# Kernel optimization log

Measured on AMD Instinct MI355X. Metric: run time of the kernel, lower is better.

## Reference

```python
import jax, jax.numpy as jnp
import numpy as np

V, H, L, B, S, T = 32000, 256, 4, 32, 64, 64


def setup_inputs() -> dict:
    key = jax.random.key(0)
    ks = jax.random.split(key, 16)
    sc = 0.05
    return {
        "encoder_outputs": jax.random.normal(ks[0], (B, S, H), jnp.float32),
        "encoder_hidden": jax.random.normal(ks[1], (L, B, H), jnp.float32),
        "decoder_input": jax.random.randint(ks[2], (B, T), 0, V),
        "embedding": jax.random.normal(ks[3], (V, H), jnp.float32) * sc,
        "Wa": jax.random.normal(ks[4], (H, H * L), jnp.float32) * sc,
        "bWa": jnp.zeros((H,), jnp.float32),
        "Ua": jax.random.normal(ks[5], (H, H), jnp.float32) * sc,
        "bUa": jnp.zeros((H,), jnp.float32),
        "Va": jax.random.normal(ks[6], (1, H), jnp.float32) * sc,
        "bVa": jnp.zeros((1,), jnp.float32),
        "W_ih0": jax.random.normal(ks[7], (3 * H, 2 * H), jnp.float32) * sc,
        "W_ih_rest": jax.random.normal(ks[8], (L - 1, 3 * H, H), jnp.float32) * sc,
        "W_hh": jax.random.normal(ks[9], (L, 3 * H, H), jnp.float32) * sc,
        "b_ih": jnp.zeros((L, 3 * H), jnp.float32),
        "b_hh": jnp.zeros((L, 3 * H), jnp.float32),
        "W_out": jax.random.normal(ks[10], (V, H), jnp.float32) * sc,
        "b_out": jnp.zeros((V,), jnp.float32),
    }


def _gru_cell(x, h, W_ih, W_hh, b_ih, b_hh):
    # PyTorch gate order: r, z, n
    gi = x @ W_ih.T + b_ih  # [B, 3H]
    gh = h @ W_hh.T + b_hh  # [B, 3H]
    ir, iz, inn = jnp.split(gi, 3, axis=-1)
    hr, hz, hn = jnp.split(gh, 3, axis=-1)
    r = jax.nn.sigmoid(ir + hr)
    z = jax.nn.sigmoid(iz + hz)
    n = jnp.tanh(inn + r * hn)
    return (1.0 - z) * n + z * h


def reference(encoder_outputs, encoder_hidden, decoder_input, embedding,
              Wa, bWa, Ua, bUa, Va, bVa,
              W_ih0, W_ih_rest, W_hh, b_ih, b_hh, W_out, b_out):
    keys = encoder_outputs  # [B,S,H]
    UaK = keys @ Ua.T + bUa  # precompute Ua(keys): [B,S,H]
    nlayers = W_hh.shape[0]

    def step(hidden, tok):
        # hidden: [L,B,H], tok: [B]
        emb = embedding[tok]  # [B,H]
        query = jnp.transpose(hidden, (1, 0, 2)).reshape(hidden.shape[1], -1)  # [B, L*H]
        e = jnp.tanh((query @ Wa.T + bWa)[:, None, :] + UaK)  # [B,S,H]
        scores = jnp.squeeze(e @ Va.T + bVa, -1)  # [B,S]
        w = jax.nn.softmax(scores, axis=-1)  # [B,S]
        ctx = jnp.einsum('bs,bsh->bh', w, keys)  # [B,H]
        x = jnp.concatenate([emb, ctx], axis=-1)  # [B,2H]
        new_h = []
        for l in range(nlayers):
            Wih = W_ih0 if l == 0 else W_ih_rest[l - 1]
            h_l = _gru_cell(x, hidden[l], Wih, W_hh[l], b_ih[l], b_hh[l])
            new_h.append(h_l)
            x = h_l
        logits = x @ W_out.T + b_out  # [B,V]
        return jnp.stack(new_h, 0), (logits, w)

    hidden_final, (logits_tbv, attn_tbs) = jax.lax.scan(step, encoder_hidden, decoder_input.T)
    logits = jnp.transpose(logits_tbv, (1, 0, 2))  # [B,T,V]
    attentions = jnp.transpose(attn_tbs, (1, 0, 2))  # [B,T,S]
    return jax.nn.log_softmax(logits, axis=-1), hidden_final, attentions
```

## Files before the change

### kernel.cpp

```cpp
#include <hip/hip_runtime.h>

typedef short s16x8 __attribute__((ext_vector_type(8)));
typedef float f32x4 __attribute__((ext_vector_type(4)));

static __device__ __forceinline__ unsigned short f2bf(float f){
  unsigned u = __builtin_bit_cast(unsigned, f);
  unsigned r = (u + 0x7fffu + ((u >> 16) & 1u)) >> 16;
  return (unsigned short)r;
}
static __device__ __forceinline__ float sigm(float x){
  return __builtin_amdgcn_rcpf(1.f + __expf(-x));
}
static __device__ __forceinline__ float tanh_(float x){
  float e = __expf(2.f * x);
  return 1.f - 2.f * __builtin_amdgcn_rcpf(e + 1.f);
}

__global__ void k_tr(const float* __restrict__ in, float* __restrict__ out, int R, int C, int ld){
  int i = blockIdx.x * 256 + threadIdx.x;
  if (i >= R * C) return;
  int c = i / R, r = i - c * R;
  out[i] = in[r * ld + c];
}

__global__ void k_wbpack(const float* __restrict__ W, unsigned short* __restrict__ Wb){
  int p = blockIdx.x * 256 + threadIdx.x;
  int j = p & 7, l = (p >> 3) & 63, ks = (p >> 9) & 7, nt = p >> 12;
  int v = nt * 16 + (l & 15);
  int k = ks * 32 + ((l >> 4) << 3) + j;
  Wb[p] = f2bf(W[v * 256 + k]);
}

__global__ void k_uak(const float* __restrict__ keys, const float* __restrict__ UaT,
                      const float* __restrict__ bUa, float* __restrict__ UaK){
  __shared__ float kl[256];
  int row = blockIdx.x, tid = threadIdx.x;
  kl[tid] = keys[row * 256 + tid];
  __syncthreads();
  float acc = bUa[tid];
  #pragma unroll 8
  for (int k = 0; k < 256; ++k) acc += kl[k] * UaT[k * 256 + tid];
  UaK[row * 256 + tid] = acc;
}

__global__ void k_gie(const int* __restrict__ tok, const float* __restrict__ emb,
                      const float* __restrict__ W0eT, const float* __restrict__ bih,
                      float* __restrict__ giE){
  __shared__ float el[256];
  int blk = blockIdx.x;
  int t = blk >> 5, b = blk & 31, tid = threadIdx.x;
  int tk = tok[b * 64 + t];
  el[tid] = emb[tk * 256 + tid];
  __syncthreads();
  for (int g = tid; g < 768; g += 256){
    float acc = bih[g];
    #pragma unroll 8
    for (int k = 0; k < 256; ++k) acc += el[k] * W0eT[k * 768 + g];
    giE[blk * 768 + g] = acc;
  }
}

__launch_bounds__(512)
__global__ void k_seq(const float* __restrict__ keys, const float* __restrict__ ehid,
                      const float* __restrict__ WaT, const float* __restrict__ bWa,
                      const float* __restrict__ Va, const float* __restrict__ bVa,
                      const float* __restrict__ UaK, const float* __restrict__ giE,
                      const float* __restrict__ W0cT, const float* __restrict__ WihT,
                      const float* __restrict__ WhhT, const float* __restrict__ bih,
                      const float* __restrict__ bhh,
                      unsigned short* __restrict__ Xb, float* __restrict__ outH,
                      float* __restrict__ outA)
{
  __shared__ float h[1024];
  __shared__ float vlds[256];
  __shared__ float qWp[1024];
  __shared__ float qW[256];
  __shared__ float ghA[3072];
  __shared__ float sc[64];
  __shared__ float watt[64];
  __shared__ float ctx[256];
  __shared__ float gi[768];
  __shared__ float red[1536];
  const int b = blockIdx.x;
  const int tid = threadIdx.x;

  for (int i = tid; i < 1024; i += 512) h[i] = ehid[(i >> 8) * 8192 + b * 256 + (i & 255)];
  if (tid < 256) vlds[tid] = Va[tid];
  __syncthreads();

  for (int t = 0; t < 64; ++t){
    #pragma unroll
    for (int pass = 0; pass < 2; ++pass){
      const int gidx = tid + pass * 512;
      const float* wp; int wstride, l, oo, isq;
      if (gidx < 256){
        isq = 1; l = gidx >> 6; oo = (gidx & 63) * 4;
        wp = WaT + l * 65536 + oo; wstride = 256;
      } else {
        isq = 0; int gid = gidx - 256; l = gid / 192; oo = (gid - l * 192) * 4;
        wp = WhhT + l * 196608 + oo; wstride = 768;
      }
      const float* xv = h + l * 256;
      float ax = 0.f, ay = 0.f, az = 0.f, aw = 0.f;
      #pragma unroll 8
      for (int k = 0; k < 256; ++k){
        float x = xv[k];
        float4 w = *(const float4*)(wp);
        ax += x * w.x; ay += x * w.y; az += x * w.z; aw += x * w.w;
        wp += wstride;
      }
      if (isq){
        float* d = qWp + l * 256 + oo;
        d[0] = ax; d[1] = ay; d[2] = az; d[3] = aw;
      } else {
        const float* bb = bhh + l * 768 + oo;
        float* d = ghA + l * 768 + oo;
        d[0] = ax + bb[0]; d[1] = ay + bb[1]; d[2] = az + bb[2]; d[3] = aw + bb[3];
      }
    }
    __syncthreads();
    if (tid < 256) qW[tid] = qWp[tid] + qWp[256 + tid] + qWp[512 + tid] + qWp[768 + tid] + bWa[tid];
    __syncthreads();

    {
      int s = tid >> 3, p = tid & 7;
      const float* up = UaK + ((b << 6) + s) * 256 + p * 32;
      const float* qp = qW + p * 32;
      const float* vp = vlds + p * 32;
      float acc = 0.f;
      #pragma unroll 8
      for (int i = 0; i < 32; ++i){
        float e = tanh_(qp[i] + up[i]);
        acc += vp[i] * e;
      }
      acc += __shfl_xor(acc, 1, 64);
      acc += __shfl_xor(acc, 2, 64);
      acc += __shfl_xor(acc, 4, 64);
      if (p == 0) sc[s] = acc + bVa[0];
    }
    __syncthreads();

    if (tid < 64){
      float v = sc[tid];
      float m = v;
      #pragma unroll
      for (int off = 1; off < 64; off <<= 1) m = fmaxf(m, __shfl_xor(m, off, 64));
      float e = __expf(v - m);
      float ssum = e;
      #pragma unroll
      for (int off = 1; off < 64; off <<= 1) ssum += __shfl_xor(ssum, off, 64);
      float w = e * __builtin_amdgcn_rcpf(ssum);
      watt[tid] = w;
      outA[(b * 64 + t) * 64 + tid] = w;
    }
    __syncthreads();

    {
      int o = tid & 255, p = tid >> 8;
      const float* kp = keys + (b * 64 + p * 32) * 256 + o;
      float acc = 0.f;
      #pragma unroll 8
      for (int s2 = 0; s2 < 32; ++s2) acc += watt[p * 32 + s2] * kp[s2 * 256];
      red[tid] = acc;
    }
    __syncthreads();
    if (tid < 256) ctx[tid] = red[tid] + red[256 + tid];
    __syncthreads();

    const float* giB = giE + (t * 32 + b) * 768;
    for (int l = 0; l < 4; ++l){
      const float* xv = (l == 0) ? ctx : (h + (l - 1) * 256);
      const float* wb = (l == 0) ? W0cT : (WihT + (l - 1) * 196608);
      if (tid < 384){
        int oo = (tid % 192) * 4, kp2 = tid / 192;
        const float* wp = wb + (kp2 * 128) * 768 + oo;
        const float* xp = xv + kp2 * 128;
        float ax = 0.f, ay = 0.f, az = 0.f, aw = 0.f;
        #pragma unroll 8
        for (int k = 0; k < 128; ++k){
          float x = xp[k];
          float4 w = *(const float4*)(wp);
          ax += x * w.x; ay += x * w.y; az += x * w.z; aw += x * w.w;
          wp += 768;
        }
        float* d = red + kp2 * 768 + oo;
        d[0] = ax; d[1] = ay; d[2] = az; d[3] = aw;
      }
      __syncthreads();
      for (int o = tid; o < 768; o += 512){
        float base = (l == 0) ? giB[o] : bih[l * 768 + o];
        gi[o] = base + red[o] + red[768 + o];
      }
      __syncthreads();
      if (tid < 256){
        int o = tid;
        const float* gh = ghA + l * 768;
        float r = sigm(gi[o] + gh[o]);
        float z = sigm(gi[256 + o] + gh[256 + o]);
        float n = tanh_(gi[512 + o] + r * gh[512 + o]);
        float hold = h[l * 256 + o];
        float hn = (1.f - z) * n + z * hold;
        h[l * 256 + o] = hn;
        if (l == 3) Xb[(b * 64 + t) * 256 + o] = f2bf(hn);
      }
      __syncthreads();
    }
  }
  for (int i = tid; i < 1024; i += 512) outH[(i >> 8) * 8192 + b * 256 + (i & 255)] = h[i];
}

__launch_bounds__(512)
__global__ void k_g1(const unsigned short* __restrict__ Xb, const unsigned short* __restrict__ Wb,
                     const float* __restrict__ bout, float* __restrict__ Spart)
{
  const int mt = blockIdx.x, nc = blockIdx.y;
  const int tid = threadIdx.x, lane = tid & 63, wv = tid >> 6;
  const int c = lane & 15, q = lane >> 4;
  const int r0 = mt * 64;
  s16x8 afr[4][8];
  #pragma unroll
  for (int rt = 0; rt < 4; ++rt){
    const unsigned short* xp = Xb + (r0 + rt * 16 + c) * 256 + q * 8;
    #pragma unroll
    for (int ks = 0; ks < 8; ++ks) afr[rt][ks] = *(const s16x8*)(xp + ks * 32);
  }
  float ssum[4][4];
  #pragma unroll
  for (int rt = 0; rt < 4; ++rt){ ssum[rt][0]=0.f; ssum[rt][1]=0.f; ssum[rt][2]=0.f; ssum[rt][3]=0.f; }
  const int ntEnd = nc * 250 + 250;
  for (int nt = nc * 250 + wv; nt < ntEnd; nt += 8){
    const unsigned short* wp = Wb + nt * 4096 + lane * 8;
    f32x4 acc[4];
    #pragma unroll
    for (int rt = 0; rt < 4; ++rt) acc[rt] = (f32x4){0.f, 0.f, 0.f, 0.f};
    #pragma unroll
    for (int ks = 0; ks < 8; ++ks){
      s16x8 bfr = *(const s16x8*)(wp + ks * 512);
      #pragma unroll
      for (int rt = 0; rt < 4; ++rt)
        acc[rt] = __builtin_amdgcn_mfma_f32_16x16x32_bf16(afr[rt][ks], bfr, acc[rt], 0, 0, 0);
    }
    float bo = bout[nt * 16 + c];
    #pragma unroll
    for (int rt = 0; rt < 4; ++rt){
      #pragma unroll
      for (int i = 0; i < 4; ++i) ssum[rt][i] += __expf(acc[rt][i] + bo);
    }
  }
  #pragma unroll
  for (int off = 1; off < 16; off <<= 1){
    #pragma unroll
    for (int rt = 0; rt < 4; ++rt){
      #pragma unroll
      for (int i = 0; i < 4; ++i) ssum[rt][i] += __shfl_xor(ssum[rt][i], off, 64);
    }
  }
  __shared__ float lred[8][64];
  if (c == 0){
    #pragma unroll
    for (int rt = 0; rt < 4; ++rt){
      #pragma unroll
      for (int i = 0; i < 4; ++i) lred[wv][rt * 16 + q * 4 + i] = ssum[rt][i];
    }
  }
  __syncthreads();
  if (tid < 64){
    float s = 0.f;
    #pragma unroll
    for (int w = 0; w < 8; ++w) s += lred[w][tid];
    Spart[(r0 + tid) * 8 + nc] = s;
  }
}

__global__ void k_g1b(const float* __restrict__ Spart, float* __restrict__ Z){
  int r = blockIdx.x * 256 + threadIdx.x;
  float s = 0.f;
  #pragma unroll
  for (int nc = 0; nc < 8; ++nc) s += Spart[r * 8 + nc];
  Z[r] = __logf(s);
}

__launch_bounds__(512)
__global__ void k_g2(const unsigned short* __restrict__ Xb, const unsigned short* __restrict__ Wb,
                     const float* __restrict__ bout, const float* __restrict__ Z,
                     float* __restrict__ out)
{
  const int mt = blockIdx.x, nc = blockIdx.y;
  const int tid = threadIdx.x, lane = tid & 63, wv = tid >> 6;
  const int c = lane & 15, q = lane >> 4;
  const int r0 = mt * 64;
  s16x8 afr[4][8];
  #pragma unroll
  for (int rt = 0; rt < 4; ++rt){
    const unsigned short* xp = Xb + (r0 + rt * 16 + c) * 256 + q * 8;
    #pragma unroll
    for (int ks = 0; ks < 8; ++ks) afr[rt][ks] = *(const s16x8*)(xp + ks * 32);
  }
  float zr[4][4];
  #pragma unroll
  for (int rt = 0; rt < 4; ++rt){
    #pragma unroll
    for (int i = 0; i < 4; ++i) zr[rt][i] = Z[r0 + rt * 16 + q * 4 + i];
  }
  const int ntEnd = nc * 250 + 250;
  for (int nt = nc * 250 + wv; nt < ntEnd; nt += 8){
    const unsigned short* wp = Wb + nt * 4096 + lane * 8;
    f32x4 acc[4];
    #pragma unroll
    for (int rt = 0; rt < 4; ++rt) acc[rt] = (f32x4){0.f, 0.f, 0.f, 0.f};
    #pragma unroll
    for (int ks = 0; ks < 8; ++ks){
      s16x8 bfr = *(const s16x8*)(wp + ks * 512);
      #pragma unroll
      for (int rt = 0; rt < 4; ++rt)
        acc[rt] = __builtin_amdgcn_mfma_f32_16x16x32_bf16(afr[rt][ks], bfr, acc[rt], 0, 0, 0);
    }
    float bo = bout[nt * 16 + c];
    #pragma unroll
    for (int rt = 0; rt < 4; ++rt){
      #pragma unroll
      for (int i = 0; i < 4; ++i)
        out[(r0 + rt * 16 + q * 4 + i) * 32000 + nt * 16 + c] = acc[rt][i] + bo - zr[rt][i];
    }
  }
}

extern "C" void kernel_launch(void* const* d_in, const int* in_sizes, int n_in,
                              void* d_out, int out_size, void* d_ws, size_t ws_size,
                              hipStream_t stream)
{
  const float* keys = (const float*)d_in[0];
  const float* ehid = (const float*)d_in[1];
  const int*   dinp = (const int*)d_in[2];
  const float* emb  = (const float*)d_in[3];
  const float* Wa   = (const float*)d_in[4];
  const float* bWa  = (const float*)d_in[5];
  const float* Ua   = (const float*)d_in[6];
  const float* bUa  = (const float*)d_in[7];
  const float* Va   = (const float*)d_in[8];
  const float* bVa  = (const float*)d_in[9];
  const float* Wih0 = (const float*)d_in[10];
  const float* Wihr = (const float*)d_in[11];
  const float* Whh  = (const float*)d_in[12];
  const float* bih  = (const float*)d_in[13];
  const float* bhh  = (const float*)d_in[14];
  const float* Wout = (const float*)d_in[15];
  const float* bout = (const float*)d_in[16];

  char* ws = (char*)d_ws;
  float* WaT   = (float*)(ws + 0);
  float* UaT   = (float*)(ws + 1048576);
  float* W0eT  = (float*)(ws + 1310720);
  float* W0cT  = (float*)(ws + 2097152);
  float* WihT  = (float*)(ws + 2883584);
  float* WhhT  = (float*)(ws + 5242880);
  float* UaK   = (float*)(ws + 8388608);
  float* giE   = (float*)(ws + 10485760);
  unsigned short* Xb = (unsigned short*)(ws + 16777216);
  unsigned short* Wb = (unsigned short*)(ws + 17825792);
  float* Spart = (float*)(ws + 34209792);
  float* Zr    = (float*)(ws + 34275328);

  float* outL = (float*)d_out;
  float* outH = outL + 65536000;
  float* outA = outH + 32768;

  k_tr<<<1024, 256, 0, stream>>>(Wa,   WaT,  256, 1024, 1024);
  k_tr<<<256,  256, 0, stream>>>(Ua,   UaT,  256, 256,  256);
  k_tr<<<768,  256, 0, stream>>>(Wih0,       W0eT, 768, 256, 512);
  k_tr<<<768,  256, 0, stream>>>(Wih0 + 256, W0cT, 768, 256, 512);
  for (int l = 0; l < 3; ++l)
    k_tr<<<768, 256, 0, stream>>>(Wihr + l * 196608, WihT + l * 196608, 768, 256, 256);
  for (int l = 0; l < 4; ++l)
    k_tr<<<768, 256, 0, stream>>>(Whh + l * 196608, WhhT + l * 196608, 768, 256, 256);

  k_wbpack<<<32000, 256, 0, stream>>>(Wout, Wb);
  k_uak<<<2048, 256, 0, stream>>>(keys, UaT, bUa, UaK);
  k_gie<<<2048, 256, 0, stream>>>(dinp, emb, W0eT, bih, giE);

  k_seq<<<32, 512, 0, stream>>>(keys, ehid, WaT, bWa, Va, bVa, UaK, giE,
                                W0cT, WihT, WhhT, bih, bhh, Xb, outH, outA);

  k_g1<<<dim3(32, 8), 512, 0, stream>>>(Xb, Wb, bout, Spart);
  k_g1b<<<8, 256, 0, stream>>>(Spart, Zr);
  k_g2<<<dim3(32, 8), 512, 0, stream>>>(Xb, Wb, bout, Zr, outL);
}
```

Measured before the change: 5.074 ms.

## Split recurrent GEMVs across blocks by output column with grid barriers and fp16 dot2

The sequential decoder kernel is restructured. Each of 32 blocks used to own one batch row and stream every weight matrix; now each block owns a slice of output columns for all batch rows. Partial results (query projection, hidden gates, input gates, context) are exchanged through global memory with software grid barriers, six per timestep. Weights and hidden state are repacked to fp16 and use the packed dot2 instruction, which halves weight traffic and lets each block's weight slice stay cache-resident. The costs are extra barrier latency and fp16 rounding of hidden state and gate values, and correctness depends on all 32 blocks being co-resident.

```diff
diff --git a/kernel.cpp b/kernel.cpp
--- a/kernel.cpp
+++ b/kernel.cpp
@@ -2,6 +2,9 @@
 
 typedef short s16x8 __attribute__((ext_vector_type(8)));
 typedef float f32x4 __attribute__((ext_vector_type(4)));
+typedef _Float16 h2 __attribute__((ext_vector_type(2)));
+typedef unsigned u32x4 __attribute__((ext_vector_type(4)));
+typedef unsigned u32x2 __attribute__((ext_vector_type(2)));
 
 static __device__ __forceinline__ unsigned short f2bf(float f){
   unsigned u = __builtin_bit_cast(unsigned, f);
@@ -14,6 +17,16 @@
 static __device__ __forceinline__ float tanh_(float x){
   float e = __expf(2.f * x);
   return 1.f - 2.f * __builtin_amdgcn_rcpf(e + 1.f);
+}
+static __device__ __forceinline__ unsigned pk2(float a, float b){
+  h2 h = { (_Float16)a, (_Float16)b };
+  return __builtin_bit_cast(unsigned, h);
+}
+static __device__ __forceinline__ h2 bch2(unsigned u){
+  return __builtin_bit_cast(h2, u);
+}
+static __device__ __forceinline__ float dot2(unsigned x, unsigned w, float acc){
+  return __builtin_amdgcn_fdot2(bch2(x), bch2(w), acc, false);
 }
 
 __global__ void k_tr(const float* __restrict__ in, float* __restrict__ out, int R, int C, int ld){
@@ -29,6 +42,24 @@
   int v = nt * 16 + (l & 15);
   int k = ks * 32 + ((l >> 4) << 3) + j;
   Wb[p] = f2bf(W[v * 256 + k]);
+}
+
+__global__ void k_packW(const float* __restrict__ src, unsigned short* __restrict__ dst,
+                        int ld, int k0){
+  int idx = blockIdx.x * 256 + threadIdx.x;
+  int g = idx >> 8, k = idx & 255;
+  int cs = g / 24, c = g - cs * 24;
+  _Float16 v = (_Float16)src[g * ld + k0 + k];
+  dst[cs * 6144 + (k >> 1) * 48 + c * 2 + (k & 1)] = __builtin_bit_cast(unsigned short, v);
+}
+
+__global__ void k_packWa(const float* __restrict__ Wa, unsigned short* __restrict__ dst){
+  int idx = blockIdx.x * 256 + threadIdx.x;
+  int c = idx >> 10, kk = idx & 1023;
+  int l = kk >> 8, k = kk & 255;
+  int cs = c >> 3, c8 = c & 7;
+  _Float16 v = (_Float16)Wa[c * 1024 + kk];
+  dst[(l * 32 + cs) * 2048 + (k >> 1) * 16 + c8 * 2 + (k & 1)] = __builtin_bit_cast(unsigned short, v);
 }
 
 __global__ void k_uak(const float* __restrict__ keys, const float* __restrict__ UaT,
@@ -60,153 +91,204 @@
   }
 }
 
-__launch_bounds__(512)
-__global__ void k_seq(const float* __restrict__ keys, const float* __restrict__ ehid,
-                      const float* __restrict__ WaT, const float* __restrict__ bWa,
-                      const float* __restrict__ Va, const float* __restrict__ bVa,
+static __device__ __forceinline__ void gridbar(int* bar, int* epoch){
+  __syncthreads();
+  if (threadIdx.x == 0){
+    ++(*epoch);
+    __hip_atomic_fetch_add(bar, 1, __ATOMIC_ACQ_REL, __HIP_MEMORY_SCOPE_AGENT);
+    const int target = 32 * (*epoch);
+    while (__hip_atomic_load(bar, __ATOMIC_ACQUIRE, __HIP_MEMORY_SCOPE_AGENT) < target)
+      __builtin_amdgcn_s_sleep(2);
+  }
+  __syncthreads();
+}
+
+__launch_bounds__(512, 1)
+__global__ void k_rec(const float* __restrict__ keys, const float* __restrict__ ehid,
+                      const unsigned short* __restrict__ WaP,
+                      const unsigned short* __restrict__ WhhP,
+                      const unsigned short* __restrict__ WihP,
+                      const float* __restrict__ bWa, const float* __restrict__ Va,
+                      const float* __restrict__ bVa,
                       const float* __restrict__ UaK, const float* __restrict__ giE,
-                      const float* __restrict__ W0cT, const float* __restrict__ WihT,
-                      const float* __restrict__ WhhT, const float* __restrict__ bih,
-                      const float* __restrict__ bhh,
+                      const float* __restrict__ bih, const float* __restrict__ bhh,
+                      float* __restrict__ qWgP, unsigned* __restrict__ ghgP,
+                      unsigned* __restrict__ gigP, unsigned* __restrict__ ctx2g,
+                      int* __restrict__ bar,
                       unsigned short* __restrict__ Xb, float* __restrict__ outH,
                       float* __restrict__ outA)
 {
-  __shared__ float h[1024];
+  __shared__ unsigned Hpk[32][4][132];
+  __shared__ unsigned Cpk[32][128];
   __shared__ float vlds[256];
-  __shared__ float qWp[1024];
-  __shared__ float qW[256];
-  __shared__ float ghA[3072];
-  __shared__ float sc[64];
-  __shared__ float watt[64];
-  __shared__ float ctx[256];
-  __shared__ float gi[768];
-  __shared__ float red[1536];
-  const int b = blockIdx.x;
+  __shared__ float qWl[256];
+  __shared__ float sc[64], watt[64];
+  __shared__ float ctxl[256];
+  __shared__ float red[512];
+  const int cs = blockIdx.x;
   const int tid = threadIdx.x;
 
-  for (int i = tid; i < 1024; i += 512) h[i] = ehid[(i >> 8) * 8192 + b * 256 + (i & 255)];
+  for (int i = tid; i < 16384; i += 512){
+    int l = i >> 12, b = (i >> 7) & 31, kp = i & 127;
+    const float* hp = ehid + l * 8192 + b * 256 + 2 * kp;
+    Hpk[b][l][kp] = pk2(hp[0], hp[1]);
+  }
   if (tid < 256) vlds[tid] = Va[tid];
   __syncthreads();
 
+  int epoch = 0;
   for (int t = 0; t < 64; ++t){
+    const int tp = t & 1;
     #pragma unroll
     for (int pass = 0; pass < 2; ++pass){
-      const int gidx = tid + pass * 512;
-      const float* wp; int wstride, l, oo, isq;
-      if (gidx < 256){
-        isq = 1; l = gidx >> 6; oo = (gidx & 63) * 4;
-        wp = WaT + l * 65536 + oo; wstride = 256;
+      const int u = pass * 512 + tid;
+      const int b = u >> 5, m = u & 31;
+      float a0, a1, a2, a3;
+      const unsigned short* wb;
+      int l, c0, wstep;
+      if (m < 8){
+        l = m >> 1; const int cg = m & 1;
+        wb = WaP + (l * 32 + cs) * 2048 + cg * 8;
+        wstep = 16; c0 = cs * 8 + cg * 4;
+        a0 = a1 = a2 = a3 = 0.f;
       } else {
-        isq = 0; int gid = gidx - 256; l = gid / 192; oo = (gid - l * 192) * 4;
-        wp = WhhT + l * 196608 + oo; wstride = 768;
+        const int mm = m - 8; l = mm / 6; const int cg = mm - l * 6;
+        wb = WhhP + (l * 32 + cs) * 6144 + cg * 8;
+        wstep = 48; c0 = cs * 24 + cg * 4;
+        const float4 bb = *(const float4*)(bhh + l * 768 + c0);
+        a0 = bb.x; a1 = bb.y; a2 = bb.z; a3 = bb.w;
       }
-      const float* xv = h + l * 256;
-      float ax = 0.f, ay = 0.f, az = 0.f, aw = 0.f;
+      const unsigned* xp = &Hpk[b][l][0];
       #pragma unroll 8
-      for (int k = 0; k < 256; ++k){
-        float x = xv[k];
-        float4 w = *(const float4*)(wp);
-        ax += x * w.x; ay += x * w.y; az += x * w.z; aw += x * w.w;
-        wp += wstride;
+      for (int kp = 0; kp < 128; ++kp){
+        u32x4 w = *(const u32x4*)(wb + kp * wstep);
+        unsigned x = xp[kp];
+        a0 = dot2(x, w.x, a0); a1 = dot2(x, w.y, a1);
+        a2 = dot2(x, w.z, a2); a3 = dot2(x, w.w, a3);
       }
-      if (isq){
-        float* d = qWp + l * 256 + oo;
-        d[0] = ax; d[1] = ay; d[2] = az; d[3] = aw;
+      if (m < 8){
+        *(f32x4*)(qWgP + (b * 4 + l) * 256 + c0) = (f32x4){a0, a1, a2, a3};
       } else {
-        const float* bb = bhh + l * 768 + oo;
-        float* d = ghA + l * 768 + oo;
-        d[0] = ax + bb[0]; d[1] = ay + bb[1]; d[2] = az + bb[2]; d[3] = aw + bb[3];
+        u32x2 o = { pk2(a0, a1), pk2(a2, a3) };
+        *(u32x2*)(ghgP + tp * 49152 + (l * 32 + b) * 384 + (c0 >> 1)) = o;
       }
     }
-    __syncthreads();
-    if (tid < 256) qW[tid] = qWp[tid] + qWp[256 + tid] + qWp[512 + tid] + qWp[768 + tid] + bWa[tid];
-    __syncthreads();
-
+    gridbar(bar, &epoch);
+
+    if (tid < 256){
+      qWl[tid] = qWgP[(cs * 4 + 0) * 256 + tid] + qWgP[(cs * 4 + 1) * 256 + tid]
+               + qWgP[(cs * 4 + 2) * 256 + tid] + qWgP[(cs * 4 + 3) * 256 + tid] + bWa[tid];
+    }
+    __syncthreads();
     {
       int s = tid >> 3, p = tid & 7;
-      const float* up = UaK + ((b << 6) + s) * 256 + p * 32;
-      const float* qp = qW + p * 32;
+      const float* up = UaK + ((cs << 6) + s) * 256 + p * 32;
+      const float* qp = qWl + p * 32;
       const float* vp = vlds + p * 32;
       float acc = 0.f;
       #pragma unroll 8
-      for (int i = 0; i < 32; ++i){
-        float e = tanh_(qp[i] + up[i]);
-        acc += vp[i] * e;
-      }
+      for (int i = 0; i < 32; ++i) acc += vp[i] * tanh_(qp[i] + up[i]);
       acc += __shfl_xor(acc, 1, 64);
       acc += __shfl_xor(acc, 2, 64);
       acc += __shfl_xor(acc, 4, 64);
       if (p == 0) sc[s] = acc + bVa[0];
     }
     __syncthreads();
-
     if (tid < 64){
       float v = sc[tid];
-      float m = v;
-      #pragma unroll
-      for (int off = 1; off < 64; off <<= 1) m = fmaxf(m, __shfl_xor(m, off, 64));
-      float e = __expf(v - m);
+      float m2 = v;
+      #pragma unroll
+      for (int off = 1; off < 64; off <<= 1) m2 = fmaxf(m2, __shfl_xor(m2, off, 64));
+      float e = __expf(v - m2);
       float ssum = e;
       #pragma unroll
       for (int off = 1; off < 64; off <<= 1) ssum += __shfl_xor(ssum, off, 64);
       float w = e * __builtin_amdgcn_rcpf(ssum);
       watt[tid] = w;
-      outA[(b * 64 + t) * 64 + tid] = w;
-    }
-    __syncthreads();
-
+      outA[(cs * 64 + t) * 64 + tid] = w;
+    }
+    __syncthreads();
     {
       int o = tid & 255, p = tid >> 8;
-      const float* kp = keys + (b * 64 + p * 32) * 256 + o;
+      const float* kp2 = keys + (cs * 64 + p * 32) * 256 + o;
       float acc = 0.f;
       #pragma unroll 8
-      for (int s2 = 0; s2 < 32; ++s2) acc += watt[p * 32 + s2] * kp[s2 * 256];
+      for (int s2 = 0; s2 < 32; ++s2) acc += watt[p * 32 + s2] * kp2[s2 * 256];
       red[tid] = acc;
     }
     __syncthreads();
-    if (tid < 256) ctx[tid] = red[tid] + red[256 + tid];
-    __syncthreads();
-
-    const float* giB = giE + (t * 32 + b) * 768;
+    if (tid < 256) ctxl[tid] = red[tid] + red[256 + tid];
+    __syncthreads();
+    if (tid < 128) ctx2g[cs * 128 + tid] = pk2(ctxl[2 * tid], ctxl[2 * tid + 1]);
+    gridbar(bar, &epoch);
+
+    for (int i = tid; i < 4096; i += 512) Cpk[i >> 7][i & 127] = ctx2g[i];
+    __syncthreads();
+
+    const int tb = t * 32;
     for (int l = 0; l < 4; ++l){
-      const float* xv = (l == 0) ? ctx : (h + (l - 1) * 256);
-      const float* wb = (l == 0) ? W0cT : (WihT + (l - 1) * 196608);
-      if (tid < 384){
-        int oo = (tid % 192) * 4, kp2 = tid / 192;
-        const float* wp = wb + (kp2 * 128) * 768 + oo;
-        const float* xp = xv + kp2 * 128;
-        float ax = 0.f, ay = 0.f, az = 0.f, aw = 0.f;
+      if (tid < 192){
+        const int b = tid / 6, cg = tid - b * 6;
+        const int c0 = cs * 24 + cg * 4;
+        const unsigned short* wb = WihP + (l * 32 + cs) * 6144 + cg * 8;
+        float a0, a1, a2, a3;
+        if (l == 0){
+          const float4 bb = *(const float4*)(giE + (tb + b) * 768 + c0);
+          a0 = bb.x; a1 = bb.y; a2 = bb.z; a3 = bb.w;
+        } else {
+          const float4 bb = *(const float4*)(bih + l * 768 + c0);
+          a0 = bb.x; a1 = bb.y; a2 = bb.z; a3 = bb.w;
+        }
+        const unsigned* xp = (l == 0) ? &Cpk[b][0] : &Hpk[b][l - 1][0];
         #pragma unroll 8
-        for (int k = 0; k < 128; ++k){
-          float x = xp[k];
-          float4 w = *(const float4*)(wp);
-          ax += x * w.x; ay += x * w.y; az += x * w.z; aw += x * w.w;
-          wp += 768;
+        for (int kp = 0; kp < 128; ++kp){
+          u32x4 w = *(const u32x4*)(wb + kp * 48);
+          unsigned x = xp[kp];
+          a0 = dot2(x, w.x, a0); a1 = dot2(x, w.y, a1);
+          a2 = dot2(x, w.z, a2); a3 = dot2(x, w.w, a3);
         }
-        float* d = red + kp2 * 768 + oo;
-        d[0] = ax; d[1] = ay; d[2] = az; d[3] = aw;
+        u32x2 o = { pk2(a0, a1), pk2(a2, a3) };
+        *(u32x2*)(gigP + l * 12288 + b * 384 + (c0 >> 1)) = o;
+      }
+      gridbar(bar, &epoch);
+      const unsigned* gl = gigP + l * 12288;
+      const unsigned* gh = ghgP + tp * 49152 + l * 32 * 384;
+      #pragma unroll
+      for (int i2 = 0; i2 < 8; ++i2){
+        const int u = tid + i2 * 512;
+        const int b = u >> 7, kp = u & 127;
+        h2 gir = bch2(gl[b * 384 + kp]);
+        h2 giz = bch2(gl[b * 384 + 128 + kp]);
+        h2 gin = bch2(gl[b * 384 + 256 + kp]);
+        h2 ghr = bch2(gh[b * 384 + kp]);
+        h2 ghz = bch2(gh[b * 384 + 128 + kp]);
+        h2 ghn = bch2(gh[b * 384 + 256 + kp]);
+        h2 hp = bch2(Hpk[b][l][kp]);
+        float hn0, hn1;
+        {
+          float r = sigm((float)gir[0] + (float)ghr[0]);
+          float z = sigm((float)giz[0] + (float)ghz[0]);
+          float n = tanh_((float)gin[0] + r * (float)ghn[0]);
+          hn0 = (1.f - z) * n + z * (float)hp[0];
+        }
+        {
+          float r = sigm((float)gir[1] + (float)ghr[1]);
+          float z = sigm((float)giz[1] + (float)ghz[1]);
+          float n = tanh_((float)gin[1] + r * (float)ghn[1]);
+          hn1 = (1.f - z) * n + z * (float)hp[1];
+        }
+        Hpk[b][l][kp] = pk2(hn0, hn1);
+        if (l == 3 && b == cs)
+          *(unsigned*)(Xb + (cs * 64 + t) * 256 + 2 * kp) =
+              (unsigned)f2bf(hn0) | ((unsigned)f2bf(hn1) << 16);
+        if (t == 63 && b == cs){
+          outH[l * 8192 + cs * 256 + 2 * kp]     = hn0;
+          outH[l * 8192 + cs * 256 + 2 * kp + 1] = hn1;
+        }
       }
       __syncthreads();
-      for (int o = tid; o < 768; o += 512){
-        float base = (l == 0) ? giB[o] : bih[l * 768 + o];
-        gi[o] = base + red[o] + red[768 + o];
-      }
-      __syncthreads();
-      if (tid < 256){
-        int o = tid;
-        const float* gh = ghA + l * 768;
-        float r = sigm(gi[o] + gh[o]);
-        float z = sigm(gi[256 + o] + gh[256 + o]);
-        float n = tanh_(gi[512 + o] + r * gh[512 + o]);
-        float hold = h[l * 256 + o];
-        float hn = (1.f - z) * n + z * hold;
-        h[l * 256 + o] = hn;
-        if (l == 3) Xb[(b * 64 + t) * 256 + o] = f2bf(hn);
-      }
-      __syncthreads();
-    }
-  }
-  for (int i = tid; i < 1024; i += 512) outH[(i >> 8) * 8192 + b * 256 + (i & 255)] = h[i];
+    }
+  }
 }
 
 __launch_bounds__(512)
@@ -347,39 +429,48 @@
   const float* Wout = (const float*)d_in[15];
   const float* bout = (const float*)d_in[16];
 
-  char* ws = (char*)d_ws;
-  float* WaT   = (float*)(ws + 0);
-  float* UaT   = (float*)(ws + 1048576);
-  float* W0eT  = (float*)(ws + 1310720);
-  float* W0cT  = (float*)(ws + 2097152);
-  float* WihT  = (float*)(ws + 2883584);
-  float* WhhT  = (float*)(ws + 5242880);
-  float* UaK   = (float*)(ws + 8388608);
-  float* giE   = (float*)(ws + 10485760);
-  unsigned short* Xb = (unsigned short*)(ws + 16777216);
-  unsigned short* Wb = (unsigned short*)(ws + 17825792);
-  float* Spart = (float*)(ws + 34209792);
-  float* Zr    = (float*)(ws + 34275328);
+  char* p = (char*)d_ws;
+  auto alloc = [&](size_t n){ char* r = p; p += (n + 255) & ~(size_t)255; return r; };
+  unsigned short* WaP  = (unsigned short*)alloc(262144 * 2);
+  unsigned short* WhhP = (unsigned short*)alloc(786432 * 2);
+  unsigned short* WihP = (unsigned short*)alloc(786432 * 2);
+  float* UaT   = (float*)alloc(65536 * 4);
+  float* W0eT  = (float*)alloc(196608 * 4);
+  float* UaK   = (float*)alloc(524288 * 4);
+  float* giE   = (float*)alloc(1572864 * 4);
+  unsigned short* Xb = (unsigned short*)alloc(524288 * 2);
+  unsigned short* Wb = (unsigned short*)alloc(8192000 * 2);
+  float* Spart = (float*)alloc(16384 * 4);
+  float* Zr    = (float*)alloc(2048 * 4);
+  float* qWgP  = (float*)alloc(32768 * 4);
+  unsigned* ghgP = (unsigned*)alloc(98304 * 4);
+  unsigned* gigP = (unsigned*)alloc(49152 * 4);
+  unsigned* ctx2g = (unsigned*)alloc(4096 * 4);
+  int* bar = (int*)alloc(256);
 
   float* outL = (float*)d_out;
   float* outH = outL + 65536000;
   float* outA = outH + 32768;
 
-  k_tr<<<1024, 256, 0, stream>>>(Wa,   WaT,  256, 1024, 1024);
-  k_tr<<<256,  256, 0, stream>>>(Ua,   UaT,  256, 256,  256);
-  k_tr<<<768,  256, 0, stream>>>(Wih0,       W0eT, 768, 256, 512);
-  k_tr<<<768,  256, 0, stream>>>(Wih0 + 256, W0cT, 768, 256, 512);
-  for (int l = 0; l < 3; ++l)
-    k_tr<<<768, 256, 0, stream>>>(Wihr + l * 196608, WihT + l * 196608, 768, 256, 256);
+  k_tr<<<256, 256, 0, stream>>>(Ua,   UaT,  256, 256, 256);
+  k_tr<<<768, 256, 0, stream>>>(Wih0, W0eT, 768, 256, 512);
+
+  k_packWa<<<1024, 256, 0, stream>>>(Wa, WaP);
   for (int l = 0; l < 4; ++l)
-    k_tr<<<768, 256, 0, stream>>>(Whh + l * 196608, WhhT + l * 196608, 768, 256, 256);
+    k_packW<<<768, 256, 0, stream>>>(Whh + l * 196608, WhhP + l * 196608, 256, 0);
+  k_packW<<<768, 256, 0, stream>>>(Wih0, WihP, 512, 256);
+  for (int l = 1; l < 4; ++l)
+    k_packW<<<768, 256, 0, stream>>>(Wihr + (l - 1) * 196608, WihP + l * 196608, 256, 0);
 
   k_wbpack<<<32000, 256, 0, stream>>>(Wout, Wb);
   k_uak<<<2048, 256, 0, stream>>>(keys, UaT, bUa, UaK);
   k_gie<<<2048, 256, 0, stream>>>(dinp, emb, W0eT, bih, giE);
 
-  k_seq<<<32, 512, 0, stream>>>(keys, ehid, WaT, bWa, Va, bVa, UaK, giE,
-                                W0cT, WihT, WhhT, bih, bhh, Xb, outH, outA);
+  hipMemsetAsync(bar, 0, 256, stream);
+
+  k_rec<<<32, 512, 0, stream>>>(keys, ehid, WaP, WhhP, WihP, bWa, Va, bVa,
+                                UaK, giE, bih, bhh,
+                                qWgP, ghgP, gigP, ctx2g, bar, Xb, outH, outA);
 
   k_g1<<<dim3(32, 8), 512, 0, stream>>>(Xb, Wb, bout, Spart);
   k_g1b<<<8, 256, 0, stream>>>(Spart, Zr);
```

Result: no change. 5.120 ms (+0.9%).
